# Optimization experiments

Hardware: AMD Instinct MI355X
Metric: run time of the kernel (lower is better)

## Reference

```python
import jax, jax.numpy as jnp
import numpy as np

B, N_ROIS, C, H, W = 4, 180, 512, 48, 48
STRIDE = 4
EPS = 1e-5


def _pool_one(feat, roi):
    # feat: [C,H,W], roi: [4] float (y1,x1,y2,x2) in image coords
    r = roi / STRIDE
    r0 = jnp.trunc(r[0]).astype(jnp.int32)
    r1 = jnp.trunc(r[1]).astype(jnp.int32)
    r2 = jnp.ceil(r[2]).astype(jnp.int32)
    r3 = jnp.ceil(r[3]).astype(jnp.int32)
    h_size = r2 - r0 + 1
    w_size = r3 - r1 + 1
    idx2 = jnp.arange(2)
    # AdaptiveMaxPool2d region boundaries: [floor(i*s/2), ceil((i+1)*s/2))
    sh = (idx2 * h_size) // 2
    eh = ((idx2 + 1) * h_size + 1) // 2
    sw = (idx2 * w_size) // 2
    ew = ((idx2 + 1) * w_size + 1) // 2
    hh = jnp.arange(H)[None, :]
    ww = jnp.arange(W)[None, :]
    mask_h = (hh >= (r0 + sh)[:, None]) & (hh < (r0 + eh)[:, None])  # [2,H]
    mask_w = (ww >= (r1 + sw)[:, None]) & (ww < (r1 + ew)[:, None])  # [2,W]
    neg = jnp.finfo(feat.dtype).min
    # max over W within each col region -> [2(oj), C, H]
    mw = jnp.where(mask_w[:, None, None, :], feat[None], neg).max(axis=-1)
    # max over H within each row region -> [2(oi), 2(oj), C]
    p = jnp.where(mask_h[:, None, None, :], mw[None], neg).max(axis=-1)
    # torch layout: [C, oi, oj] then flatten row-major
    return jnp.transpose(p, (2, 0, 1)).reshape(-1)  # [C*4]


def _roi_pool(features, rois):
    # features: [B,C,H,W], rois: [B,N,4] -> [B,N,C*4]
    def per_roi(roi_b):  # roi_b: [B,4]
        return jax.vmap(_pool_one)(features, roi_b)  # [B, C*4]
    out = jax.lax.map(per_roi, jnp.swapaxes(rois, 0, 1))  # [N,B,C*4]
    return jnp.swapaxes(out, 0, 1)


def _bn(x, gamma, beta):
    # training-mode BatchNorm1d over [B, N_ROIS(channels), F]: stats over (B,F)
    mean = x.mean(axis=(0, 2), keepdims=True)
    var = ((x - mean) ** 2).mean(axis=(0, 2), keepdims=True)
    return (x - mean) * jax.lax.rsqrt(var + EPS) * gamma[None, :, None] + beta[None, :, None]


def setup_inputs() -> dict:
    key = jax.random.key(0)
    k1, k2, k3, k4, k5 = jax.random.split(key, 5)
    features = jax.random.normal(k1, (B, C, H, W), dtype=jnp.float32)
    max_coord = (H - 1) * STRIDE
    y = jnp.sort(jax.random.uniform(k2, (B, N_ROIS, 2), minval=0.0, maxval=max_coord), axis=-1)
    x = jnp.sort(jax.random.uniform(k3, (B, N_ROIS, 2), minval=0.0, maxval=max_coord), axis=-1)
    rois = jnp.stack([y[..., 0], x[..., 0], y[..., 1], x[..., 1]], axis=-1)  # [B,N,4]
    F_in = C * 4
    W1 = jax.random.normal(k4, (64, F_in), dtype=jnp.float32) * 0.02
    bl1 = jnp.zeros((64,), dtype=jnp.float32)
    gamma1 = jnp.ones((N_ROIS,), dtype=jnp.float32)
    beta1 = jnp.zeros((N_ROIS,), dtype=jnp.float32)
    gamma2 = jnp.ones((N_ROIS,), dtype=jnp.float32)
    beta2 = jnp.zeros((N_ROIS,), dtype=jnp.float32)
    return {"features": features, "rois": rois, "gamma1": gamma1, "beta1": beta1,
            "W1": W1, "bl1": bl1, "gamma2": gamma2, "beta2": beta2}


def reference(features, rois, gamma1, beta1, W1, bl1, gamma2, beta2):
    pooled = _roi_pool(features, rois)            # [B, 180, 2048]
    x = jax.nn.relu(pooled)
    x = _bn(x, gamma1, beta1)
    y = jnp.einsum('bnf,of->bno', x, W1) + bl1    # [B, 180, 64]
    y = _bn(y, gamma2, beta2)
    return y
```

## Files before the change

kernel.cpp:

```cpp
#include <hip/hip_runtime.h>
#include <hip/hip_bf16.h>
#include <cfloat>
#include <math.h>

#define BB 4
#define NR 180
#define CC 512
#define HH 48
#define WW 48
#define FF (CC*4)
#define OO 64
#define EPSV 1e-5f
#define NCH 4


typedef unsigned short us2 __attribute__((ext_vector_type(2)));

__device__ __forceinline__ unsigned pmax(unsigned a, unsigned b) {
    return __builtin_bit_cast(unsigned, __builtin_elementwise_max(
        __builtin_bit_cast(us2, a), __builtin_bit_cast(us2, b)));
}
__device__ __forceinline__ uint4 pmax4(uint4 a, uint4 b) {
    return make_uint4(pmax(a.x,b.x), pmax(a.y,b.y), pmax(a.z,b.z), pmax(a.w,b.w));
}
__device__ __forceinline__ unsigned mapb(float f) {
    unsigned fu = __float_as_uint(f);
    unsigned u = fu >> 16;
    return (fu >> 31) ? (~u & 0xFFFFu) : (u | 0x8000u);
}
__device__ __forceinline__ void unmap2(unsigned m, float& lo, float& hi) {
    unsigned t = ((~m) >> 15) & 0x00010001u;
    unsigned u = m ^ (0x80008000u ^ (t * 0x7FFFu));
    lo = __uint_as_float(u << 16);
    hi = __uint_as_float(u & 0xffff0000u);
}

__global__ __launch_bounds__(256) void k_prep(const float* __restrict__ feat,
                                              const float* __restrict__ W1,
                                              ushort* __restrict__ featB,
                                              float* __restrict__ W1T4) {
    __shared__ float tile[32][33];
    int t = threadIdx.x;
    int L = blockIdx.x;

    if (L < 4608) {
        const int S = HH * WW;
        int xcd = L & 7;
        int b   = xcd >> 1;
        int m   = ((L >> 3) << 1) | (xcd & 1);
        int s0  = (m % 72) * 32;
        int c0  = (m / 72) * 32;
        const float* src = feat + (size_t)b * CC * S;
        ushort* dst = featB + (size_t)b * S * CC;

        int cl = t >> 3;
        int sx = (t & 7) << 2;
        float4 v = *(const float4*)(src + (size_t)(c0 + cl) * S + s0 + sx);
        tile[cl][sx] = v.x; tile[cl][sx+1] = v.y; tile[cl][sx+2] = v.z; tile[cl][sx+3] = v.w;
        __syncthreads();

        int sl = t >> 3;
        int c4 = (t & 7) << 2;
        unsigned u0 = mapb(tile[c4][sl])   | (mapb(tile[c4+1][sl]) << 16);
        unsigned u1 = mapb(tile[c4+2][sl]) | (mapb(tile[c4+3][sl]) << 16);
        *(uint2*)(dst + (size_t)(s0 + sl) * CC + c0 + c4) = make_uint2(u0, u1);
    } else {
        int kt = L - 4608;
        int k0 = (kt >> 1) * 32, o0 = (kt & 1) * 32;
        int tx = t & 31, ty = t >> 5;
        #pragma unroll
        for (int k = 0; k < 4; k++) {
            int row = ty + k * 8;
            tile[row][tx] = W1[(size_t)(o0 + row) * FF + (k0 + tx)];
        }
        __syncthreads();
        #pragma unroll
        for (int k = 0; k < 4; k++) {
            int row = ty + k * 8;
            int kk = k0 + row;
            int o  = o0 + tx;
            W1T4[(size_t)(kk >> 2) * 256 + o * 4 + (kk & 3)] = tile[tx][row];
        }
    }
}

__global__ __launch_bounds__(256, 6) void k_pool(const ushort* __restrict__ featB,
                                                 const float* __restrict__ rois,
                                                 ushort* __restrict__ pp) {
    __shared__ unsigned lu[4][16][64];
    int L = blockIdx.x;
    int xcd = L & 7;
    int b   = xcd >> 1;
    int tt  = L >> 3;
    int ch  = ((xcd & 1) << 1) | (tt & 1);
    int n   = tt >> 1;
    int tid = threadIdx.x;
    int g = tid >> 6, c = tid & 63;

    const float* roi = rois + ((size_t)b * NR + n) * 4;
    int r0 = (int)(roi[0] * 0.25f);
    int r1 = (int)(roi[1] * 0.25f);
    int r2 = (int)ceilf(roi[2] * 0.25f);
    int r3 = (int)ceilf(roi[3] * 0.25f);
    int hs  = r2 - r0 + 1;
    int wsz = r3 - r1 + 1;
    int eh0 = (hs + 1) >> 1, sh1 = hs >> 1;
    int ew0 = (wsz + 1) >> 1, sw1 = wsz >> 1;

    const uint4 Z = make_uint4(0,0,0,0);
    uint4 q00 = Z, q01 = Z, q10 = Z, q11 = Z;

    for (int Lr = ch * 4 + g; Lr < hs; Lr += 16) {
        const uint4* rp = (const uint4*)(featB + ((size_t)((b * HH + r0 + Lr) * WW + r1)) * CC) + c;
        uint4 cm0 = Z, cm1 = Z;
        {
            int e = ew0 - 1;
            for (int w = 0; w < ew0; w += 8) {
                uint4 u0 = rp[(size_t)64 * w];
                uint4 u1 = rp[(size_t)64 * min(w + 1, e)];
                uint4 u2 = rp[(size_t)64 * min(w + 2, e)];
                uint4 u3 = rp[(size_t)64 * min(w + 3, e)];
                uint4 u4 = rp[(size_t)64 * min(w + 4, e)];
                uint4 u5 = rp[(size_t)64 * min(w + 5, e)];
                uint4 u6 = rp[(size_t)64 * min(w + 6, e)];
                uint4 u7 = rp[(size_t)64 * min(w + 7, e)];
                cm0 = pmax4(cm0, pmax4(pmax4(pmax4(u0,u1), pmax4(u2,u3)),
                                       pmax4(pmax4(u4,u5), pmax4(u6,u7))));
            }
        }
        {
            int e = wsz - 1;
            for (int w = sw1; w < wsz; w += 8) {
                uint4 u0 = rp[(size_t)64 * w];
                uint4 u1 = rp[(size_t)64 * min(w + 1, e)];
                uint4 u2 = rp[(size_t)64 * min(w + 2, e)];
                uint4 u3 = rp[(size_t)64 * min(w + 3, e)];
                uint4 u4 = rp[(size_t)64 * min(w + 4, e)];
                uint4 u5 = rp[(size_t)64 * min(w + 5, e)];
                uint4 u6 = rp[(size_t)64 * min(w + 6, e)];
                uint4 u7 = rp[(size_t)64 * min(w + 7, e)];
                cm1 = pmax4(cm1, pmax4(pmax4(pmax4(u0,u1), pmax4(u2,u3)),
                                       pmax4(pmax4(u4,u5), pmax4(u6,u7))));
            }
        }
        if (Lr <  eh0) { q00 = pmax4(q00, cm0); q01 = pmax4(q01, cm1); }
        if (Lr >= sh1) { q10 = pmax4(q10, cm0); q11 = pmax4(q11, cm1); }
    }

    {
        unsigned a, b2;
        a = q00.x; b2 = q01.x;
        lu[g][0*4 + 0][c] = (a & 0xFFFFu) | (b2 << 16);
        lu[g][0*4 + 2][c] = (a >> 16)     | (b2 & 0xFFFF0000u);
        a = q10.x; b2 = q11.x;
        lu[g][0*4 + 1][c] = (a & 0xFFFFu) | (b2 << 16);
        lu[g][0*4 + 3][c] = (a >> 16)     | (b2 & 0xFFFF0000u);
        a = q00.y; b2 = q01.y;
        lu[g][1*4 + 0][c] = (a & 0xFFFFu) | (b2 << 16);
        lu[g][1*4 + 2][c] = (a >> 16)     | (b2 & 0xFFFF0000u);
        a = q10.y; b2 = q11.y;
        lu[g][1*4 + 1][c] = (a & 0xFFFFu) | (b2 << 16);
        lu[g][1*4 + 3][c] = (a >> 16)     | (b2 & 0xFFFF0000u);
        a = q00.z; b2 = q01.z;
        lu[g][2*4 + 0][c] = (a & 0xFFFFu) | (b2 << 16);
        lu[g][2*4 + 2][c] = (a >> 16)     | (b2 & 0xFFFF0000u);
        a = q10.z; b2 = q11.z;
        lu[g][2*4 + 1][c] = (a & 0xFFFFu) | (b2 << 16);
        lu[g][2*4 + 3][c] = (a >> 16)     | (b2 & 0xFFFF0000u);
        a = q00.w; b2 = q01.w;
        lu[g][3*4 + 0][c] = (a & 0xFFFFu) | (b2 << 16);
        lu[g][3*4 + 2][c] = (a >> 16)     | (b2 & 0xFFFF0000u);
        a = q10.w; b2 = q11.w;
        lu[g][3*4 + 1][c] = (a & 0xFFFFu) | (b2 << 16);
        lu[g][3*4 + 3][c] = (a >> 16)     | (b2 & 0xFFFF0000u);
    }
    __syncthreads();

    int c2 = tid & 63, j0 = (tid >> 6) * 4;
    unsigned ou[4];
    #pragma unroll
    for (int jj = 0; jj < 4; jj++) {
        int j = j0 + jj;
        unsigned m = pmax(pmax(lu[0][j][c2], lu[1][j][c2]),
                          pmax(lu[2][j][c2], lu[3][j][c2]));
        ou[jj] = pmax(m, 0x80008000u);
    }
    unsigned* dst = (unsigned*)(pp + ((size_t)(b * NR + n) * NCH + ch) * FF);
    *(uint4*)(dst + c2 * 16 + j0) = make_uint4(ou[0], ou[1], ou[2], ou[3]);
}

__global__ __launch_bounds__(1024) void k_gemm(const ushort* __restrict__ pp,
                                               const float* __restrict__ W1T4,
                                               const float* __restrict__ bl1,
                                               const float* __restrict__ g1,
                                               const float* __restrict__ b1,
                                               const float* __restrict__ g2,
                                               const float* __restrict__ b2,
                                               float* __restrict__ out) {
    __shared__ float xs[BB][FF];
    __shared__ float pd[16][BB][OO];
    __shared__ float pw[16][OO];
    __shared__ float part_s[16], part_q[16];
    __shared__ float sm2[4], sq2[4];
    int n = blockIdx.x;
    int tid = threadIdx.x;

    float s_acc = 0.f, q_acc = 0.f;
    #pragma unroll
    for (int k2 = 0; k2 < 2; k2++) {
        int gi = tid + (k2 << 10);
        int bb = gi >> 9;
        int idx = gi & 511;
        const unsigned* base = (const unsigned*)(pp + ((size_t)(bb * NR + n)) * NCH * FF);
        uint2 m = *(const uint2*)(base + 0 * (FF / 2) + idx * 2);
        #pragma unroll
        for (int cch = 1; cch < NCH; cch++) {
            uint2 u = *(const uint2*)(base + cch * (FF / 2) + idx * 2);
            m.x = pmax(m.x, u.x);
            m.y = pmax(m.y, u.y);
        }
        float v0, v1, v2, v3;
        unmap2(m.x, v0, v1);
        unmap2(m.y, v2, v3);
        *(float4*)&xs[bb][idx << 2] = make_float4(v0, v1, v2, v3);
        s_acc += v0 + v1 + v2 + v3;
        q_acc += v0*v0 + v1*v1 + v2*v2 + v3*v3;
    }
    for (int off = 32; off; off >>= 1) {
        s_acc += __shfl_down(s_acc, off);
        q_acc += __shfl_down(q_acc, off);
    }
    if ((tid & 63) == 0) { part_s[tid >> 6] = s_acc; part_q[tid >> 6] = q_acc; }
    __syncthreads();
    float ts = 0.f, tq = 0.f;
    #pragma unroll
    for (int i = 0; i < 16; i++) { ts += part_s[i]; tq += part_q[i]; }
    const float inv1 = 1.f / (float)(BB * FF);
    float mean = ts * inv1;
    float var  = tq * inv1 - mean * mean;
    float a1n  = g1[n] * rsqrtf(var + EPSV);
    float c1n  = b1[n] - mean * a1n;

    int sc = tid >> 6;
    int o  = tid & 63;
    int k4a = sc << 5;
    float a0 = 0.f, a1 = 0.f, a2 = 0.f, a3 = 0.f, wsum = 0.f;
    #pragma unroll 4
    for (int k4 = k4a; k4 < k4a + 32; k4++) {
        float4 w4 = *(const float4*)(W1T4 + (size_t)k4 * 256 + o * 4);
        float4 x0 = *(const float4*)&xs[0][k4 << 2];
        float4 x1 = *(const float4*)&xs[1][k4 << 2];
        float4 x2 = *(const float4*)&xs[2][k4 << 2];
        float4 x3 = *(const float4*)&xs[3][k4 << 2];
        wsum += w4.x + w4.y + w4.z + w4.w;
        a0 += w4.x*x0.x + w4.y*x0.y + w4.z*x0.z + w4.w*x0.w;
        a1 += w4.x*x1.x + w4.y*x1.y + w4.z*x1.z + w4.w*x1.w;
        a2 += w4.x*x2.x + w4.y*x2.y + w4.z*x2.z + w4.w*x2.w;
        a3 += w4.x*x3.x + w4.y*x3.y + w4.z*x3.z + w4.w*x3.w;
    }
    pd[sc][0][o] = a0; pd[sc][1][o] = a1; pd[sc][2][o] = a2; pd[sc][3][o] = a3;
    pw[sc][o] = wsum;
    __syncthreads();

    float y = 0.f;
    int b = tid >> 6;
    if (tid < 256) {
        float dot = 0.f, wsm = 0.f;
        #pragma unroll
        for (int ss = 0; ss < 16; ss++) { dot += pd[ss][b][o]; wsm += pw[ss][o]; }
        y = a1n * dot + c1n * wsm + bl1[o];
        float rs = y, rq = y * y;
        for (int off = 32; off; off >>= 1) {
            rs += __shfl_down(rs, off);
            rq += __shfl_down(rq, off);
        }
        if (o == 0) { sm2[b] = rs; sq2[b] = rq; }
    }
    __syncthreads();
    if (tid < 256) {
        float sm  = sm2[0] + sm2[1] + sm2[2] + sm2[3];
        float sqm = sq2[0] + sq2[1] + sq2[2] + sq2[3];
        const float inv2 = 1.f / 256.f;
        float mean2 = sm * inv2;
        float var2  = sqm * inv2 - mean2 * mean2;
        float r2s = rsqrtf(var2 + EPSV);
        out[((size_t)b * NR + n) * OO + o] = (y - mean2) * r2s * g2[n] + b2[n];
    }
}

extern "C" void kernel_launch(void* const* d_in, const int* in_sizes, int n_in,
                              void* d_out, int out_size, void* d_ws, size_t ws_size,
                              hipStream_t stream) {
    const float* feat = (const float*)d_in[0];
    const float* rois = (const float*)d_in[1];
    const float* g1   = (const float*)d_in[2];
    const float* b1   = (const float*)d_in[3];
    const float* W1   = (const float*)d_in[4];
    const float* bl1  = (const float*)d_in[5];
    const float* g2   = (const float*)d_in[6];
    const float* b2   = (const float*)d_in[7];
    float* out = (float*)d_out;

    ushort* featB = (ushort*)d_ws;
    float*  W1T4  = (float*)(featB + (size_t)BB*HH*WW*CC);
    ushort* pp    = (ushort*)(W1T4 + (size_t)OO*FF);

    k_prep<<<4736, 256, 0, stream>>>(feat, W1, featB, W1T4);
    k_pool<<<2880, 256, 0, stream>>>(featB, rois, pp);
    k_gemm<<<NR, 1024, 0, stream>>>(pp, W1T4, bl1, g1, b1, g2, b2, out);
}
```

Before: 117.9 us.

## Split ROI pooling into per-row column-max and per-ROI row-max kernels

Replaces the single ROI pooling kernel with two stages. The first stages one feature row (all W and C) in shared memory per block and computes the two column-region maxima for every ROI that covers that row. The second reduces those over the ROI's row ranges. This removes redundant global re-reads of overlapping feature rows and the 4-way channel-chunk partial outputs merged in the GEMM. In exchange it adds an extra kernel launch and a colmax intermediate written and read through global memory. It also drops the XCD-aware block mapping.

```diff
diff --git a/kernel.cpp b/kernel.cpp
--- a/kernel.cpp
+++ b/kernel.cpp
@@ -11,7 +11,6 @@
 #define FF (CC*4)
 #define OO 64
 #define EPSV 1e-5f
-#define NCH 4
 
 
 typedef unsigned short us2 __attribute__((ext_vector_type(2)));
@@ -45,9 +44,8 @@
 
     if (L < 4608) {
         const int S = HH * WW;
-        int xcd = L & 7;
-        int b   = xcd >> 1;
-        int m   = ((L >> 3) << 1) | (xcd & 1);
+        int b   = L & 3;
+        int m   = L >> 2;
         int s0  = (m % 72) * 32;
         int c0  = (m / 72) * 32;
         const float* src = feat + (size_t)b * CC * S;
@@ -84,67 +82,84 @@
     }
 }
 
-__global__ __launch_bounds__(256, 6) void k_pool(const ushort* __restrict__ featB,
-                                                 const float* __restrict__ rois,
-                                                 ushort* __restrict__ pp) {
+__global__ __launch_bounds__(512) void k_colmax(const ushort* __restrict__ featB,
+                                                const float* __restrict__ rois,
+                                                ushort* __restrict__ colmax) {
+    __shared__ uint4 row[48 * 64];
+    __shared__ int4 meta[NR];
+    int b = blockIdx.x & 3;
+    int h = blockIdx.x >> 2;
+    int t = threadIdx.x;
+
+    if (t < NR) {
+        float4 r = ((const float4*)(rois))[b * NR + t];
+        int r0 = (int)(r.x * 0.25f);
+        int r1 = (int)(r.y * 0.25f);
+        int r2 = (int)ceilf(r.z * 0.25f);
+        int r3 = (int)ceilf(r.w * 0.25f);
+        int wsz = r3 - r1 + 1;
+        int ew0 = (wsz + 1) >> 1, sw1 = wsz >> 1;
+        meta[t] = make_int4(r0, r2, r1, ew0 | (sw1 << 8) | (wsz << 16));
+    }
+    {
+        const uint4* src = (const uint4*)(featB + ((size_t)(b * HH + h) * WW) * CC);
+        #pragma unroll
+        for (int i = 0; i < 6; i++) row[t + 512 * i] = src[t + 512 * i];
+    }
+    __syncthreads();
+
+    int wv = t >> 6, lane = t & 63;
+    for (int n = wv; n < NR; n += 8) {
+        int4 m = meta[n];
+        if (h < m.x || h > m.y) continue;
+        int r1  = m.z;
+        int ew0 = m.w & 255;
+        int sw1 = (m.w >> 8) & 255;
+        int wsz = m.w >> 16;
+
+        uint4 s0 = make_uint4(0,0,0,0);
+        {
+            int w = r1, e = r1 + ew0;
+            for (; w + 2 <= e; w += 2)
+                s0 = pmax4(s0, pmax4(row[w * 64 + lane], row[(w + 1) * 64 + lane]));
+            if (w < e) s0 = pmax4(s0, row[w * 64 + lane]);
+        }
+        uint4 s1 = make_uint4(0,0,0,0);
+        {
+            int w = r1 + sw1, e = r1 + wsz;
+            for (; w + 2 <= e; w += 2)
+                s1 = pmax4(s1, pmax4(row[w * 64 + lane], row[(w + 1) * 64 + lane]));
+            if (w < e) s1 = pmax4(s1, row[w * 64 + lane]);
+        }
+        uint4* dst = (uint4*)((unsigned*)(colmax) + ((size_t)(b * NR + n) * 48 + h) * 512);
+        dst[lane]      = s0;
+        dst[64 + lane] = s1;
+    }
+}
+
+__global__ __launch_bounds__(256) void k_rowmax(const ushort* __restrict__ colmax,
+                                                const float* __restrict__ rois,
+                                                ushort* __restrict__ pp) {
     __shared__ unsigned lu[4][16][64];
-    int L = blockIdx.x;
-    int xcd = L & 7;
-    int b   = xcd >> 1;
-    int tt  = L >> 3;
-    int ch  = ((xcd & 1) << 1) | (tt & 1);
-    int n   = tt >> 1;
+    int b = blockIdx.x & 3;
+    int n = blockIdx.x >> 2;
     int tid = threadIdx.x;
     int g = tid >> 6, c = tid & 63;
 
     const float* roi = rois + ((size_t)b * NR + n) * 4;
     int r0 = (int)(roi[0] * 0.25f);
-    int r1 = (int)(roi[1] * 0.25f);
     int r2 = (int)ceilf(roi[2] * 0.25f);
-    int r3 = (int)ceilf(roi[3] * 0.25f);
     int hs  = r2 - r0 + 1;
-    int wsz = r3 - r1 + 1;
     int eh0 = (hs + 1) >> 1, sh1 = hs >> 1;
-    int ew0 = (wsz + 1) >> 1, sw1 = wsz >> 1;
-
-    const uint4 Z = make_uint4(0,0,0,0);
-    uint4 q00 = Z, q01 = Z, q10 = Z, q11 = Z;
-
-    for (int Lr = ch * 4 + g; Lr < hs; Lr += 16) {
-        const uint4* rp = (const uint4*)(featB + ((size_t)((b * HH + r0 + Lr) * WW + r1)) * CC) + c;
-        uint4 cm0 = Z, cm1 = Z;
-        {
-            int e = ew0 - 1;
-            for (int w = 0; w < ew0; w += 8) {
-                uint4 u0 = rp[(size_t)64 * w];
-                uint4 u1 = rp[(size_t)64 * min(w + 1, e)];
-                uint4 u2 = rp[(size_t)64 * min(w + 2, e)];
-                uint4 u3 = rp[(size_t)64 * min(w + 3, e)];
-                uint4 u4 = rp[(size_t)64 * min(w + 4, e)];
-                uint4 u5 = rp[(size_t)64 * min(w + 5, e)];
-                uint4 u6 = rp[(size_t)64 * min(w + 6, e)];
-                uint4 u7 = rp[(size_t)64 * min(w + 7, e)];
-                cm0 = pmax4(cm0, pmax4(pmax4(pmax4(u0,u1), pmax4(u2,u3)),
-                                       pmax4(pmax4(u4,u5), pmax4(u6,u7))));
-            }
-        }
-        {
-            int e = wsz - 1;
-            for (int w = sw1; w < wsz; w += 8) {
-                uint4 u0 = rp[(size_t)64 * w];
-                uint4 u1 = rp[(size_t)64 * min(w + 1, e)];
-                uint4 u2 = rp[(size_t)64 * min(w + 2, e)];
-                uint4 u3 = rp[(size_t)64 * min(w + 3, e)];
-                uint4 u4 = rp[(size_t)64 * min(w + 4, e)];
-                uint4 u5 = rp[(size_t)64 * min(w + 5, e)];
-                uint4 u6 = rp[(size_t)64 * min(w + 6, e)];
-                uint4 u7 = rp[(size_t)64 * min(w + 7, e)];
-                cm1 = pmax4(cm1, pmax4(pmax4(pmax4(u0,u1), pmax4(u2,u3)),
-                                       pmax4(pmax4(u4,u5), pmax4(u6,u7))));
-            }
-        }
-        if (Lr <  eh0) { q00 = pmax4(q00, cm0); q01 = pmax4(q01, cm1); }
-        if (Lr >= sh1) { q10 = pmax4(q10, cm0); q11 = pmax4(q11, cm1); }
+
+    uint4 q00 = make_uint4(0,0,0,0), q01 = q00, q10 = q00, q11 = q00;
+    const unsigned* base = (const unsigned*)(colmax) + ((size_t)(b * NR + n) * 48 + r0) * 512;
+    for (int hr = g; hr < hs; hr += 4) {
+        const uint4* rw = (const uint4*)(base + (size_t)hr * 512);
+        uint4 s0 = rw[c];
+        uint4 s1 = rw[64 + c];
+        if (hr <  eh0) { q00 = pmax4(q00, s0); q01 = pmax4(q01, s1); }
+        if (hr >= sh1) { q10 = pmax4(q10, s0); q11 = pmax4(q11, s1); }
     }
 
     {
@@ -185,7 +200,7 @@
                           pmax(lu[2][j][c2], lu[3][j][c2]));
         ou[jj] = pmax(m, 0x80008000u);
     }
-    unsigned* dst = (unsigned*)(pp + ((size_t)(b * NR + n) * NCH + ch) * FF);
+    unsigned* dst = (unsigned*)(pp + (size_t)(b * NR + n) * FF);
     *(uint4*)(dst + c2 * 16 + j0) = make_uint4(ou[0], ou[1], ou[2], ou[3]);
 }
 
@@ -211,14 +226,8 @@
         int gi = tid + (k2 << 10);
         int bb = gi >> 9;
         int idx = gi & 511;
-        const unsigned* base = (const unsigned*)(pp + ((size_t)(bb * NR + n)) * NCH * FF);
-        uint2 m = *(const uint2*)(base + 0 * (FF / 2) + idx * 2);
-        #pragma unroll
-        for (int cch = 1; cch < NCH; cch++) {
-            uint2 u = *(const uint2*)(base + cch * (FF / 2) + idx * 2);
-            m.x = pmax(m.x, u.x);
-            m.y = pmax(m.y, u.y);
-        }
+        const uint2* base = (const uint2*)(pp + (size_t)(bb * NR + n) * FF);
+        uint2 m = base[idx];
         float v0, v1, v2, v3;
         unmap2(m.x, v0, v1);
         unmap2(m.y, v2, v3);
@@ -301,11 +310,13 @@
     const float* b2   = (const float*)d_in[7];
     float* out = (float*)d_out;
 
-    ushort* featB = (ushort*)d_ws;
-    float*  W1T4  = (float*)(featB + (size_t)BB*HH*WW*CC);
-    ushort* pp    = (ushort*)(W1T4 + (size_t)OO*FF);
+    ushort* featB  = (ushort*)d_ws;
+    float*  W1T4   = (float*)((char*)d_ws + 9437184);
+    ushort* pp     = (ushort*)((char*)d_ws + 9961472);
+    ushort* colmax = (ushort*)((char*)d_ws + 12910592);
 
     k_prep<<<4736, 256, 0, stream>>>(feat, W1, featB, W1T4);
-    k_pool<<<2880, 256, 0, stream>>>(featB, rois, pp);
+    k_colmax<<<192, 512, 0, stream>>>(featB, rois, colmax);
+    k_rowmax<<<720, 256, 0, stream>>>(colmax, rois, pp);
     k_gemm<<<NR, 1024, 0, stream>>>(pp, W1T4, bl1, g1, b1, g2, b2, out);
 }
```

New measurement: 119.9 us. About the same (+1.7%).
